# Performance work log

Measured on AMD Instinct MI355X. Metric: run time of the kernel, lower is better.

The kernel has to match this reference:

```python
import jax, jax.numpy as jnp
import numpy as np


def setup_inputs() -> dict:
    key = jax.random.key(0)
    x = jax.random.normal(key, (256, 1024), dtype=jnp.float32)
    return {"x": x}


def reference(x):
    # SelMul: for input row [a, b, c] output is [a*a, a*b, a*c, b*b, b*c, c*c],
    # i.e. x[:, i] * x[:, j] for all i <= j, in row-major upper-triangular order.
    # The torch original materializes the full n^2 outer product then slices;
    # here we gather only the n(n+1)/2 needed pairs directly.
    n = x.shape[-1]
    rows, cols = jnp.triu_indices(n)  # rows[k] <= cols[k], row-major order
    return x[:, rows] * x[:, cols]  # (B, n*(n+1)//2)
```

## Files before the change

### kernel.cpp

```cpp
#include <hip/hip_runtime.h>


#define N 1024
#define TRI (N * (N + 1) / 2)
#define TPB 256
#define PAIRS 64
#define CHUNKS (N / 2 / PAIRS)
#define NBLOCKS (256 * CHUNKS)

__device__ __forceinline__ void row_copy(float* __restrict__ outb,
                                         const float* __restrict__ sx,
                                         int i, int t) {
    const int L = N - i;
    const int rs = (i * (2 * N + 1 - i)) >> 1;
    const float xi = sx[i];
    float* const dst = outb + rs;

    int h = (4 - (rs & 3)) & 3;
    h = (h < L) ? h : L;
    if (t < h) dst[t] = xi * sx[i + t];

    const int nb4 = (L - h) >> 2;
    for (int m = t; m < nb4; m += TPB) {
        const int k = h + (m << 2);
        const float* __restrict__ s = sx + i + k;
        float4 v;
        v.x = xi * s[0];
        v.y = xi * s[1];
        v.z = xi * s[2];
        v.w = xi * s[3];
        *reinterpret_cast<float4*>(dst + k) = v;
    }

    const int tail = (L - h) & 3;
    if (t < tail) {
        const int k = h + (nb4 << 2) + t;
        dst[k] = xi * sx[i + k];
    }
}

__global__ __launch_bounds__(TPB) void selmul_kernel(const float* __restrict__ x,
                                                     float* __restrict__ out) {
    __shared__ float sx[N];
    const int b = blockIdx.x / CHUNKS;
    const int c = blockIdx.x % CHUNKS;
    const int t = threadIdx.x;

    reinterpret_cast<float4*>(sx)[t] =
        reinterpret_cast<const float4*>(x + b * N)[t];
    __syncthreads();

    float* const outb = out + (size_t)b * TRI;
    const int i0 = c * PAIRS;
#pragma unroll 1
    for (int p = 0; p < PAIRS; ++p) {
        const int i = i0 + p;
        row_copy(outb, sx, i, t);
        row_copy(outb, sx, (N - 1) - i, t);
    }
}

extern "C" void kernel_launch(void* const* d_in, const int* in_sizes, int n_in,
                              void* d_out, int out_size, void* d_ws, size_t ws_size,
                              hipStream_t stream) {
    const float* x = (const float*)d_in[0];
    float* out = (float*)d_out;
    selmul_kernel<<<NBLOCKS, TPB, 0, stream>>>(x, out);
}
```

Baseline: 608.1 us.

## Assign row pairs per wavefront, read x from global, use nontemporal stores

Each 64-lane wavefront now owns a pair of triangle rows (i, N-1-i), replacing the block-wide loop that staged the input row in shared memory. Source values are read straight from global memory, where they should hit in cache. Misalignment between source and destination is handled with shifted float4 loads chosen by a switch. Output is written with nontemporal stores so the large write-once stream does not pollute the cache, and the __syncthreads and LDS traffic go away. In exchange, every load goes to global/L2 instead of LDS, and the kernel adds switch branching plus extra vector loads for the shifted cases.

```diff
diff --git a/kernel.cpp b/kernel.cpp
--- a/kernel.cpp
+++ b/kernel.cpp
@@ -4,59 +4,82 @@
 #define N 1024
 #define TRI (N * (N + 1) / 2)
 #define TPB 256
-#define PAIRS 64
-#define CHUNKS (N / 2 / PAIRS)
-#define NBLOCKS (256 * CHUNKS)
+#define NBLOCKS 2048
+#define NWAVES (NBLOCKS * (TPB / 64))
+#define NJOBS (256 * 512)
+#define JOBS_PER_WAVE (NJOBS / NWAVES)
 
-__device__ __forceinline__ void row_copy(float* __restrict__ outb,
-                                         const float* __restrict__ sx,
-                                         int i, int t) {
+typedef float vf4 __attribute__((ext_vector_type(4)));
+
+__device__ __forceinline__ void do_row(const float* __restrict__ xrow,
+                                       float* __restrict__ outb,
+                                       int i, int lane) {
     const int L = N - i;
     const int rs = (i * (2 * N + 1 - i)) >> 1;
-    const float xi = sx[i];
+    const float xi = xrow[i];
     float* const dst = outb + rs;
+    const float* const src = xrow + i;
 
-    int h = (4 - (rs & 3)) & 3;
-    h = (h < L) ? h : L;
-    if (t < h) dst[t] = xi * sx[i + t];
+    int h = (-rs) & 3;
+    h = h < L ? h : L;
+    const int d = (i + h) & 3;
+    const int base = (i + h) - d;
+    int nb4 = (L - h) >> 2;
+    if (d && nb4) --nb4;
 
-    const int nb4 = (L - h) >> 2;
-    for (int m = t; m < nb4; m += TPB) {
-        const int k = h + (m << 2);
-        const float* __restrict__ s = sx + i + k;
-        float4 v;
-        v.x = xi * s[0];
-        v.y = xi * s[1];
-        v.z = xi * s[2];
-        v.w = xi * s[3];
-        *reinterpret_cast<float4*>(dst + k) = v;
+    if (lane < h) dst[lane] = xi * src[lane];
+
+    const vf4* __restrict__ s4 = reinterpret_cast<const vf4*>(xrow + base);
+    vf4* const d4 = reinterpret_cast<vf4*>(dst + h);
+
+    switch (d) {
+    case 0:
+        for (int m = lane; m < nb4; m += 64) {
+            const vf4 a = s4[m];
+            __builtin_nontemporal_store(xi * a, &d4[m]);
+        }
+        break;
+    case 1:
+        for (int m = lane; m < nb4; m += 64) {
+            const vf4 a = s4[m], b = s4[m + 1];
+            vf4 o; o.x = a.y; o.y = a.z; o.z = a.w; o.w = b.x;
+            __builtin_nontemporal_store(xi * o, &d4[m]);
+        }
+        break;
+    case 2:
+        for (int m = lane; m < nb4; m += 64) {
+            const vf4 a = s4[m], b = s4[m + 1];
+            vf4 o; o.x = a.z; o.y = a.w; o.z = b.x; o.w = b.y;
+            __builtin_nontemporal_store(xi * o, &d4[m]);
+        }
+        break;
+    default:
+        for (int m = lane; m < nb4; m += 64) {
+            const vf4 a = s4[m], b = s4[m + 1];
+            vf4 o; o.x = a.w; o.y = b.x; o.z = b.y; o.w = b.z;
+            __builtin_nontemporal_store(xi * o, &d4[m]);
+        }
+        break;
     }
 
-    const int tail = (L - h) & 3;
-    if (t < tail) {
-        const int k = h + (nb4 << 2) + t;
-        dst[k] = xi * sx[i + k];
-    }
+    const int done = h + (nb4 << 2);
+    const int k = done + lane;
+    if (k < L) dst[k] = xi * src[k];
 }
 
 __global__ __launch_bounds__(TPB) void selmul_kernel(const float* __restrict__ x,
                                                      float* __restrict__ out) {
-    __shared__ float sx[N];
-    const int b = blockIdx.x / CHUNKS;
-    const int c = blockIdx.x % CHUNKS;
-    const int t = threadIdx.x;
-
-    reinterpret_cast<float4*>(sx)[t] =
-        reinterpret_cast<const float4*>(x + b * N)[t];
-    __syncthreads();
-
-    float* const outb = out + (size_t)b * TRI;
-    const int i0 = c * PAIRS;
+    const int w = (blockIdx.x * TPB + threadIdx.x) >> 6;
+    const int lane = threadIdx.x & 63;
 #pragma unroll 1
-    for (int p = 0; p < PAIRS; ++p) {
-        const int i = i0 + p;
-        row_copy(outb, sx, i, t);
-        row_copy(outb, sx, (N - 1) - i, t);
+    for (int k = 0; k < JOBS_PER_WAVE; ++k) {
+        const int q = w + k * NWAVES;
+        const int b = q >> 9;
+        const int ip = q & 511;
+        const float* xrow = x + b * N;
+        float* outb = out + (size_t)b * TRI;
+        do_row(xrow, outb, ip, lane);
+        do_row(xrow, outb, (N - 1) - ip, lane);
     }
 }
 
```

Result: faster. 576.3 us (-5.2%).

## Use shifted LDS copies for aligned vector reads and per-wave row assignment

Applied to the files above, without the earlier changes.

Stores four shifted copies of the input row in shared memory so each output row's products can be read as aligned 16-byte vectors instead of four scalar LDS loads. Work is also split so each 64-lane wave handles its own 16 row pairs independently rather than the whole block cooperating on every row. This cuts LDS instruction count and block-wide divergence per row. In exchange it uses four times the shared memory and a longer staging loop, and per-wave work can be uneven across rows.

```diff
diff --git a/kernel.cpp b/kernel.cpp
--- a/kernel.cpp
+++ b/kernel.cpp
@@ -4,59 +4,68 @@
 #define N 1024
 #define TRI (N * (N + 1) / 2)
 #define TPB 256
-#define PAIRS 64
-#define CHUNKS (N / 2 / PAIRS)
+#define CHUNKS 8
 #define NBLOCKS (256 * CHUNKS)
+#define PAIRS_PER_WAVE 16
 
-__device__ __forceinline__ void row_copy(float* __restrict__ outb,
-                                         const float* __restrict__ sx,
-                                         int i, int t) {
-    const int L = N - i;
-    const int rs = (i * (2 * N + 1 - i)) >> 1;
-    const float xi = sx[i];
-    float* const dst = outb + rs;
-
-    int h = (4 - (rs & 3)) & 3;
-    h = (h < L) ? h : L;
-    if (t < h) dst[t] = xi * sx[i + t];
-
-    const int nb4 = (L - h) >> 2;
-    for (int m = t; m < nb4; m += TPB) {
-        const int k = h + (m << 2);
-        const float* __restrict__ s = sx + i + k;
-        float4 v;
-        v.x = xi * s[0];
-        v.y = xi * s[1];
-        v.z = xi * s[2];
-        v.w = xi * s[3];
-        *reinterpret_cast<float4*>(dst + k) = v;
-    }
-
-    const int tail = (L - h) & 3;
-    if (t < tail) {
-        const int k = h + (nb4 << 2) + t;
-        dst[k] = xi * sx[i + k];
-    }
-}
+typedef float vf4 __attribute__((ext_vector_type(4)));
 
 __global__ __launch_bounds__(TPB) void selmul_kernel(const float* __restrict__ x,
                                                      float* __restrict__ out) {
-    __shared__ float sx[N];
+    __shared__ float sx[4][N];
+
     const int b = blockIdx.x / CHUNKS;
-    const int c = blockIdx.x % CHUNKS;
-    const int t = threadIdx.x;
+    const int chunk = blockIdx.x % CHUNKS;
+    const int tid = threadIdx.x;
+    const int wv = tid >> 6;
+    const int lane = tid & 63;
 
-    reinterpret_cast<float4*>(sx)[t] =
-        reinterpret_cast<const float4*>(x + b * N)[t];
+    const float* __restrict__ xrow = x + b * N;
+
+#pragma unroll
+    for (int c = 0; c < 4; ++c) {
+        for (int t = tid; t < N; t += TPB) {
+            const int g = t + c;
+            sx[c][t] = (g < N) ? xrow[g] : 0.0f;
+        }
+    }
     __syncthreads();
 
     float* const outb = out + (size_t)b * TRI;
-    const int i0 = c * PAIRS;
+    const int ip0 = chunk * 64 + wv * PAIRS_PER_WAVE;
+
 #pragma unroll 1
-    for (int p = 0; p < PAIRS; ++p) {
-        const int i = i0 + p;
-        row_copy(outb, sx, i, t);
-        row_copy(outb, sx, (N - 1) - i, t);
+    for (int p = 0; p < PAIRS_PER_WAVE; ++p) {
+        const int ipair = ip0 + p;
+#pragma unroll
+        for (int half = 0; half < 2; ++half) {
+            const int i = half ? (N - 1) - ipair : ipair;
+            const int L = N - i;
+            const int rs = (i * (2 * N + 1 - i)) >> 1;
+            const float xi = sx[0][i];
+            float* const dst = outb + rs;
+
+            int h = (-rs) & 3;
+            h = h < L ? h : L;
+            const int s = i + h;
+            const int d = s & 3;
+            const int nb4 = (L - h) >> 2;
+
+            if (lane < h) dst[lane] = xi * sx[0][i + lane];
+
+            const vf4* __restrict__ lsrc =
+                reinterpret_cast<const vf4*>(&sx[d][s - d]);
+            vf4* const d4 = reinterpret_cast<vf4*>(dst + h);
+
+            for (int m = lane; m < nb4; m += 64) {
+                const vf4 a = lsrc[m];
+                d4[m] = xi * a;
+            }
+
+            const int done = h + (nb4 << 2);
+            const int k = done + lane;
+            if (k < L) dst[k] = xi * sx[0][i + k];
+        }
     }
 }
 
```

Result: faster. 548.7 us (-9.8%).
